# Optimization experiments

Hardware: AMD Instinct MI355X
Metric: run time of the kernel (lower is better)

Reference implementation:

```python
import jax, jax.numpy as jnp
import numpy as np

R = 2  # p-norm order, matches init kwarg r=2
NUM_CLASSES = 13  # hardcoded in the original forward


def setup_inputs() -> dict:
    key = jax.random.key(0)
    k1, k2, k3, k4, k5 = jax.random.split(key, 5)
    N = 262144
    inp = jax.random.uniform(k1, (N, NUM_CLASSES), dtype=jnp.float32)
    target = jax.random.randint(k2, (N,), 0, NUM_CLASSES, dtype=jnp.int64)
    s = jax.random.normal(k3, (N, NUM_CLASSES), dtype=jnp.float32)
    C_matrix = jax.random.normal(k4, (N, NUM_CLASSES, NUM_CLASSES), dtype=jnp.float32)
    instance_weights = jax.random.uniform(k5, (N,), dtype=jnp.float32)
    return {"input": inp, "target": target, "s": s, "C_matrix": C_matrix,
            "instance_weights": instance_weights}


def _pnorm(x, r, axis):
    # torch.norm(x, r, dim) for float r: (sum |x|^r)^(1/r)
    return jnp.sum(jnp.abs(x) ** r, axis=axis) ** (1.0 / r)


def reference(input, target, s, C_matrix, instance_weights):
    # one-hot scatter of targets: p[n, target[n]] = 1
    p = jax.nn.one_hot(target, NUM_CLASSES, dtype=input.dtype)  # [N,13]
    # batched matvec: C_matrix [N,13,13] @ p [N,13] -> [N,13]
    z_pe = jnp.einsum('nij,nj->ni', C_matrix, p)
    z_p = s - z_pe
    z_p_norm = _pnorm(z_p, R, axis=1)  # [N]
    z_ye = jnp.einsum('nij,nj->ni', C_matrix, input)
    z_y = s - z_ye
    z_y_norm = _pnorm(z_y, R, axis=1)  # [N]
    # diag(z_y @ z_p^T) == row-wise dot product (original wastefully builds NxN)
    diag = jnp.sum(z_y * z_p, axis=1)  # [N]
    return jnp.sum(z_p_norm - diag / z_y_norm)
```

## Files before the change

kernel.cpp:

```cpp
#include <hip/hip_runtime.h>
#include <hip/hip_bf16.h>

#define NCLS 13
#define ROWS 16
#define BLOCK 256
#define TPB 8
#define C_FLOATS (ROWS * NCLS * NCLS)
#define XS_FLOATS (ROWS * NCLS)
#define C_F4 (C_FLOATS / 4)
#define XS_F4 (XS_FLOATS / 4)

__device__ __forceinline__ void async_cp16(const float* g, float* l) {
    __builtin_amdgcn_global_load_lds(
        (__attribute__((address_space(1))) void*)(const_cast<float*>(g)),
        (__attribute__((address_space(3))) void*)(l),
        16, 0, 0);
}

__device__ __forceinline__ void stage_tile(float* cb, float* xb, float* sb,
                                           const float* __restrict__ C,
                                           const float* __restrict__ input,
                                           const float* __restrict__ s,
                                           int tile, int tid) {
    const float* Cg = C + (size_t)tile * C_FLOATS;
    async_cp16(Cg + (size_t)tid * 4,         cb + (size_t)tid * 4);
    async_cp16(Cg + (size_t)(tid + 256) * 4, cb + (size_t)(tid + 256) * 4);
    if (tid < C_F4 - 512)
        async_cp16(Cg + (size_t)(tid + 512) * 4, cb + (size_t)(tid + 512) * 4);
    if (tid < XS_F4)
        async_cp16(input + (size_t)tile * XS_FLOATS + (size_t)tid * 4,
                   xb + (size_t)tid * 4);
    else if (tid >= 64 && tid < 64 + XS_F4)
        async_cp16(s + (size_t)tile * XS_FLOATS + (size_t)(tid - 64) * 4,
                   sb + (size_t)(tid - 64) * 4);
}

__global__ __launch_bounds__(BLOCK) void rnorm_kernel(
    const float* __restrict__ input,
    const int* __restrict__ target,
    const float* __restrict__ s,
    const float* __restrict__ C,
    float* __restrict__ out,
    int ntiles)
{
    __shared__ __align__(16) float cbuf[2][C_FLOATS];
    __shared__ __align__(16) float xbuf[2][XS_FLOATS];
    __shared__ __align__(16) float sbuf[2][XS_FLOATS];
    __shared__ float wsum[4];

    const int tid = threadIdx.x;
    const int row = tid >> 4;
    const int q   = tid & 15;

    const int tile0 = blockIdx.x * TPB;
    const int nt = min(TPB, ntiles - tile0);
    float res_acc = 0.0f;

    if (nt > 0) {
        stage_tile(cbuf[0], xbuf[0], sbuf[0], C, input, s, tile0, tid);
        int t_cur = target[tile0 * ROWS + row];
        asm volatile("s_waitcnt vmcnt(0)" ::: "memory");
        __syncthreads();

        for (int t = 0; t < nt; ++t) {
            const int cur = t & 1;
            const float* cb = cbuf[cur];
            const float* xb = xbuf[cur];
            const float* sb = sbuf[cur];

            int t_next = 0;
            if (t + 1 < nt) {
                stage_tile(cbuf[cur ^ 1], xbuf[cur ^ 1], sbuf[cur ^ 1],
                           C, input, s, tile0 + t + 1, tid);
                t_next = target[(tile0 + t + 1) * ROWS + row];
            }

            float sp = 0.0f, sy = 0.0f, dd = 0.0f;
            if (q < NCLS) {
                const float* crow = cb + row * (NCLS * NCLS) + q * NCLS;
                const float* xrow = xb + row * NCLS;
                float zye = 0.0f;
#pragma unroll
                for (int j = 0; j < NCLS; ++j)
                    zye = fmaf(crow[j], xrow[j], zye);
                const float zpe = crow[t_cur];
                const float svi = sb[row * NCLS + q];
                const float zp = svi - zpe, zy = svi - zye;
                sp = zp * zp;
                sy = zy * zy;
                dd = zy * zp;
            }

            sp += __shfl_xor(sp, 1); sp += __shfl_xor(sp, 2);
            sp += __shfl_xor(sp, 4); sp += __shfl_xor(sp, 8);
            sy += __shfl_xor(sy, 1); sy += __shfl_xor(sy, 2);
            sy += __shfl_xor(sy, 4); sy += __shfl_xor(sy, 8);
            dd += __shfl_xor(dd, 1); dd += __shfl_xor(dd, 2);
            dd += __shfl_xor(dd, 4); dd += __shfl_xor(dd, 8);

            if (q == 0)
                res_acc += sqrtf(sp) - dd / sqrtf(sy);

            if (t + 1 < nt) {
                asm volatile("s_waitcnt vmcnt(0)" ::: "memory");
                __syncthreads();
                t_cur = t_next;
            }
        }
    }

#pragma unroll
    for (int off = 32; off > 0; off >>= 1)
        res_acc += __shfl_down(res_acc, off, 64);

    const int lane = tid & 63;
    const int wid  = tid >> 6;
    if (lane == 0) wsum[wid] = res_acc;
    __syncthreads();
    if (tid == 0)
        atomicAdd(out, wsum[0] + wsum[1] + wsum[2] + wsum[3]);
}

extern "C" void kernel_launch(void* const* d_in, const int* in_sizes, int n_in,
                              void* d_out, int out_size, void* d_ws, size_t ws_size,
                              hipStream_t stream) {
    const float* input  = (const float*)d_in[0];
    const int*   target = (const int*)d_in[1];
    const float* s      = (const float*)d_in[2];
    const float* C      = (const float*)d_in[3];

    float* out = (float*)d_out;
    int N = in_sizes[1];

    hipMemsetAsync(out, 0, sizeof(float) * out_size, stream);

    const int ntiles = N / ROWS;
    const int grid = (ntiles + TPB - 1) / TPB;
    rnorm_kernel<<<grid, BLOCK, 0, stream>>>(input, target, s, C, out, ntiles);
}
```

Measured before the change: 60.16 us.

## Triple-buffer LDS staging with prefetch distance two and async target loads

Replaces the double-buffered staging with a three-buffer ring that prefetches two tiles ahead, using partial vmcnt waits so only the oldest stage must finish before each barrier. Each wave now stages its own contiguous slice of the C tile. Target indices also move into LDS through async copies instead of per-thread global loads. Tiles per block double, which halves the grid, and the larger LDS footprint may lower occupancy in exchange for more bytes in flight per block.

```diff
diff --git a/kernel.cpp b/kernel.cpp
--- a/kernel.cpp
+++ b/kernel.cpp
@@ -4,35 +4,18 @@
 #define NCLS 13
 #define ROWS 16
 #define BLOCK 256
-#define TPB 8
+#define TPB 16
+#define NBUF 3
 #define C_FLOATS (ROWS * NCLS * NCLS)
 #define XS_FLOATS (ROWS * NCLS)
-#define C_F4 (C_FLOATS / 4)
-#define XS_F4 (XS_FLOATS / 4)
+#define CW 676
+#define CW4 169
 
 __device__ __forceinline__ void async_cp16(const float* g, float* l) {
     __builtin_amdgcn_global_load_lds(
         (__attribute__((address_space(1))) void*)(const_cast<float*>(g)),
         (__attribute__((address_space(3))) void*)(l),
         16, 0, 0);
-}
-
-__device__ __forceinline__ void stage_tile(float* cb, float* xb, float* sb,
-                                           const float* __restrict__ C,
-                                           const float* __restrict__ input,
-                                           const float* __restrict__ s,
-                                           int tile, int tid) {
-    const float* Cg = C + (size_t)tile * C_FLOATS;
-    async_cp16(Cg + (size_t)tid * 4,         cb + (size_t)tid * 4);
-    async_cp16(Cg + (size_t)(tid + 256) * 4, cb + (size_t)(tid + 256) * 4);
-    if (tid < C_F4 - 512)
-        async_cp16(Cg + (size_t)(tid + 512) * 4, cb + (size_t)(tid + 512) * 4);
-    if (tid < XS_F4)
-        async_cp16(input + (size_t)tile * XS_FLOATS + (size_t)tid * 4,
-                   xb + (size_t)tid * 4);
-    else if (tid >= 64 && tid < 64 + XS_F4)
-        async_cp16(s + (size_t)tile * XS_FLOATS + (size_t)(tid - 64) * 4,
-                   sb + (size_t)(tid - 64) * 4);
 }
 
 __global__ __launch_bounds__(BLOCK) void rnorm_kernel(
@@ -43,52 +26,79 @@
     float* __restrict__ out,
     int ntiles)
 {
-    __shared__ __align__(16) float cbuf[2][C_FLOATS];
-    __shared__ __align__(16) float xbuf[2][XS_FLOATS];
-    __shared__ __align__(16) float sbuf[2][XS_FLOATS];
+    __shared__ __align__(16) float cb[NBUF][C_FLOATS];
+    __shared__ __align__(16) float xb[NBUF][XS_FLOATS];
+    __shared__ __align__(16) float sb[NBUF][XS_FLOATS];
+    __shared__ __align__(16) int   tb[NBUF][ROWS];
     __shared__ float wsum[4];
 
-    const int tid = threadIdx.x;
-    const int row = tid >> 4;
-    const int q   = tid & 15;
+    const int tid  = threadIdx.x;
+    const int w    = tid >> 6;
+    const int lane = tid & 63;
+    const int row  = tid >> 4;
+    const int q    = tid & 15;
 
     const int tile0 = blockIdx.x * TPB;
     const int nt = min(TPB, ntiles - tile0);
     float res_acc = 0.0f;
 
+    auto stage = [&](int t_idx, int buf) {
+        const int tile = tile0 + t_idx;
+        const float4* Cg = (const float4*)(C + (size_t)tile * C_FLOATS) + w * CW4;
+        float* cd = &cb[buf][w * CW];
+        async_cp16((const float*)(Cg + lane),       cd + (size_t)lane * 4);
+        async_cp16((const float*)(Cg + 64 + lane),  cd + (size_t)(64 + lane) * 4);
+        if (lane < CW4 - 128)
+            async_cp16((const float*)(Cg + 128 + lane), cd + (size_t)(128 + lane) * 4);
+        if (w == 0) {
+            const float4* xg = (const float4*)(input + (size_t)tile * XS_FLOATS);
+            if (lane < XS_FLOATS / 4)
+                async_cp16((const float*)(xg + lane), &xb[buf][0] + (size_t)lane * 4);
+        } else if (w == 1) {
+            const float4* sg = (const float4*)(s + (size_t)tile * XS_FLOATS);
+            if (lane < XS_FLOATS / 4)
+                async_cp16((const float*)(sg + lane), &sb[buf][0] + (size_t)lane * 4);
+        } else {
+            if (lane < ROWS / 4)
+                async_cp16((const float*)(target + (size_t)tile * ROWS) + (size_t)lane * 4,
+                           (float*)&tb[buf][0] + (size_t)lane * 4);
+        }
+    };
+
     if (nt > 0) {
-        stage_tile(cbuf[0], xbuf[0], sbuf[0], C, input, s, tile0, tid);
-        int t_cur = target[tile0 * ROWS + row];
-        asm volatile("s_waitcnt vmcnt(0)" ::: "memory");
-        __syncthreads();
+        stage(0, 0);
+        if (nt > 1) {
+            stage(1, 1);
+            asm volatile("s_waitcnt vmcnt(4)" ::: "memory");
+        } else {
+            asm volatile("s_waitcnt vmcnt(0)" ::: "memory");
+        }
+        __builtin_amdgcn_s_barrier();
 
+        int bcur = 0;
         for (int t = 0; t < nt; ++t) {
-            const int cur = t & 1;
-            const float* cb = cbuf[cur];
-            const float* xb = xbuf[cur];
-            const float* sb = sbuf[cur];
+            if (t + 2 < nt) {
+                int bpre = bcur + 2; if (bpre >= NBUF) bpre -= NBUF;
+                stage(t + 2, bpre);
+            }
 
-            int t_next = 0;
-            if (t + 1 < nt) {
-                stage_tile(cbuf[cur ^ 1], xbuf[cur ^ 1], sbuf[cur ^ 1],
-                           C, input, s, tile0 + t + 1, tid);
-                t_next = target[(tile0 + t + 1) * ROWS + row];
-            }
+            const float* cbt = cb[bcur];
+            const float* xbt = xb[bcur];
+            const float* sbt = sb[bcur];
+            const int tt = tb[bcur][row];
 
             float sp = 0.0f, sy = 0.0f, dd = 0.0f;
             if (q < NCLS) {
-                const float* crow = cb + row * (NCLS * NCLS) + q * NCLS;
-                const float* xrow = xb + row * NCLS;
+                const float* crow = cbt + row * (NCLS * NCLS) + q * NCLS;
+                const float* xrow = xbt + row * NCLS;
                 float zye = 0.0f;
 #pragma unroll
                 for (int j = 0; j < NCLS; ++j)
                     zye = fmaf(crow[j], xrow[j], zye);
-                const float zpe = crow[t_cur];
-                const float svi = sb[row * NCLS + q];
+                const float zpe = crow[tt];
+                const float svi = sbt[row * NCLS + q];
                 const float zp = svi - zpe, zy = svi - zye;
-                sp = zp * zp;
-                sy = zy * zy;
-                dd = zy * zp;
+                sp = zp * zp; sy = zy * zy; dd = zy * zp;
             }
 
             sp += __shfl_xor(sp, 1); sp += __shfl_xor(sp, 2);
@@ -102,10 +112,11 @@
                 res_acc += sqrtf(sp) - dd / sqrtf(sy);
 
             if (t + 1 < nt) {
-                asm volatile("s_waitcnt vmcnt(0)" ::: "memory");
-                __syncthreads();
-                t_cur = t_next;
+                if (t + 2 < nt) asm volatile("s_waitcnt vmcnt(4)" ::: "memory");
+                else            asm volatile("s_waitcnt vmcnt(0)" ::: "memory");
+                __builtin_amdgcn_s_barrier();
             }
+            bcur = (bcur + 1 == NBUF) ? 0 : bcur + 1;
         }
     }
 
@@ -113,9 +124,7 @@
     for (int off = 32; off > 0; off >>= 1)
         res_acc += __shfl_down(res_acc, off, 64);
 
-    const int lane = tid & 63;
-    const int wid  = tid >> 6;
-    if (lane == 0) wsum[wid] = res_acc;
+    if (lane == 0) wsum[w] = res_acc;
     __syncthreads();
     if (tid == 0)
         atomicAdd(out, wsum[0] + wsum[1] + wsum[2] + wsum[3]);
```

Result: faster. 50.83 us (-15.5%).
